# Kernel optimization log

Measured on AMD Instinct MI355X. Metric: run time of the kernel, lower is better.

Reference implementation:

```python
import jax, jax.numpy as jnp
import numpy as np

DIM = 1024
NUM_HEADS = 16
HEAD_DIM = DIM // NUM_HEADS


def setup_inputs() -> dict:
    key = jax.random.key(0)
    ks = jax.random.split(key, 8)
    B, N = 4, 1024
    x = jax.random.normal(ks[0], (B, N, DIM), dtype=jnp.float32)
    # RoPE tables per position, broadcast over batch/heads
    pos = jnp.arange(N, dtype=jnp.float32)[:, None]
    inv_freq = 1.0 / (10000.0 ** (jnp.arange(0, HEAD_DIM, 2, dtype=jnp.float32) / HEAD_DIM))
    ang = pos * inv_freq[None, :]                      # [N, D/2]
    ang = jnp.concatenate([ang, ang], axis=-1)          # [N, D]
    cos, sin = jnp.cos(ang), jnp.sin(ang)
    s_in = 1.0 / np.sqrt(DIM)
    qkv_w = jax.random.normal(ks[1], (3 * DIM, DIM), dtype=jnp.float32) * s_in
    qkv_b = jax.random.normal(ks[2], (3 * DIM,), dtype=jnp.float32) * 0.02
    proj_w = jax.random.normal(ks[3], (DIM, DIM), dtype=jnp.float32) * s_in
    proj_b = jax.random.normal(ks[4], (DIM,), dtype=jnp.float32) * 0.02
    return {"x": x, "cos": cos, "sin": sin, "qkv_w": qkv_w, "qkv_b": qkv_b,
            "proj_w": proj_w, "proj_b": proj_b}


def _rotate_half(t):
    t1, t2 = jnp.split(t, 2, axis=-1)
    return jnp.concatenate([-t2, t1], axis=-1)


def reference(x, cos, sin, qkv_w, qkv_b, proj_w, proj_b):
    B, N, C = x.shape
    H, D = NUM_HEADS, HEAD_DIM
    scale = D ** -0.5
    qkv = x @ qkv_w.T + qkv_b                           # [B, N, 3C]
    qkv = qkv.reshape(B, N, 3, H, D).transpose(2, 0, 3, 1, 4)  # [3, B, H, N, D]
    q, k, v = qkv[0], qkv[1], qkv[2]
    q = q * cos + _rotate_half(q) * sin                 # cos/sin [N, D] broadcast
    k = k * cos + _rotate_half(k) * sin
    attn = jnp.einsum('bhnd,bhmd->bhnm', q, k) * scale  # [B, H, N, N]
    attn = jax.nn.softmax(attn, axis=-1)
    out = jnp.einsum('bhnm,bhmd->bhnd', attn, v)        # [B, H, N, D]
    out = out.transpose(0, 2, 1, 3).reshape(B, N, C)
    return out @ proj_w.T + proj_b
```

## Files before the change

### kernel.cpp

```cpp
#include <hip/hip_runtime.h>

typedef __attribute__((ext_vector_type(8))) short bf16x8;
typedef __attribute__((ext_vector_type(4))) float f32x4;
typedef __attribute__((ext_vector_type(4))) unsigned short us4;

#define LOG2E 1.44269504088896f
#define GP(p) (const __attribute__((address_space(1))) void*)(p)
#define LP(p) (__attribute__((address_space(3))) void*)(p)

__device__ inline unsigned short f2bf(float f) {
    unsigned u = __float_as_uint(f);
    u += 0x7fffu + ((u >> 16) & 1u);
    return (unsigned short)(u >> 16);
}

__device__ inline unsigned cvt_pk_bf16(float lo, float hi) {
    unsigned r;
    asm("v_cvt_pk_bf16_f32 %0, %1, %2" : "=v"(r) : "v"(lo), "v"(hi));
    return r;
}

__global__ void cvt3_kernel(const float* __restrict__ x, const float* __restrict__ qw,
                            const float* __restrict__ pw,
                            unsigned short* __restrict__ xb, unsigned short* __restrict__ wqkv,
                            unsigned short* __restrict__ wproj) {
    const int nthreads = gridDim.x * blockDim.x;
    for (int i = blockIdx.x * blockDim.x + threadIdx.x; i < 2097152; i += nthreads) {
        const float* src; unsigned short* dst; int off;
        if (i < 1048576)      { src = x;  dst = xb;    off = i; }
        else if (i < 1835008) { src = qw; dst = wqkv;  off = i - 1048576; }
        else                  { src = pw; dst = wproj; off = i - 1835008; }
        const float4 v = *reinterpret_cast<const float4*>(src + off * 4);
        us4 o;
        o.x = f2bf(v.x); o.y = f2bf(v.y); o.z = f2bf(v.z); o.w = f2bf(v.w);
        *reinterpret_cast<us4*>(dst + off * 4) = o;
    }
}

__device__ inline void gemm_mainloop_db(const unsigned short* __restrict__ A,
                                        const unsigned short* __restrict__ Bw,
                                        unsigned short* As, unsigned short* Bs,
                                        int tm, int tn, f32x4 (&acc)[4][4]) {
    const int K = 1024;
    const int tid = threadIdx.x;
    const int lane = tid & 63;
    const int wv = tid >> 6;
    const int wr = wv >> 1, wc = wv & 1;
    const int lr = lane & 15, lg = lane >> 4;

    const int c1 = tid, c2 = tid + 256;
    const int r1 = c1 >> 2, r2 = c2 >> 2;
    const int g1 = ((c1 & 3) ^ ((r1 >> 1) & 3)) * 8;
    const int g2 = ((c2 & 3) ^ ((r2 >> 1) & 3)) * 8;
    const unsigned short* Ag1 = A + (size_t)(tm * 128 + r1) * K + g1;
    const unsigned short* Ag2 = A + (size_t)(tm * 128 + r2) * K + g2;
    const unsigned short* Bg1 = Bw + (size_t)(tn * 128 + r1) * K + g1;
    const unsigned short* Bg2 = Bw + (size_t)(tn * 128 + r2) * K + g2;

    const int rs = (lr >> 1) & 3;

    auto STAGE = [&](int buf, int k0) {
        __builtin_amdgcn_global_load_lds(GP(Ag1 + k0), LP(As + buf * 4096 + c1 * 8), 16, 0, 0);
        __builtin_amdgcn_global_load_lds(GP(Ag2 + k0), LP(As + buf * 4096 + c2 * 8), 16, 0, 0);
        __builtin_amdgcn_global_load_lds(GP(Bg1 + k0), LP(Bs + buf * 4096 + c1 * 8), 16, 0, 0);
        __builtin_amdgcn_global_load_lds(GP(Bg2 + k0), LP(Bs + buf * 4096 + c2 * 8), 16, 0, 0);
    };

    STAGE(0, 0);
    for (int t = 0; t < 32; t++) {
        const int buf = t & 1;
        if (t < 31) {
            STAGE(buf ^ 1, (t + 1) * 32);
            asm volatile("s_waitcnt vmcnt(4)" ::: "memory");
        } else {
            asm volatile("s_waitcnt vmcnt(0)" ::: "memory");
        }
        __builtin_amdgcn_s_barrier();
        __builtin_amdgcn_sched_barrier(0);

        bf16x8 af[4], bfv[4];
#pragma unroll
        for (int i = 0; i < 4; i++) {
            const int sl = (lg ^ rs) * 8;
            af[i]  = *reinterpret_cast<const bf16x8*>(As + buf * 4096 + (wr * 64 + i * 16 + lr) * 32 + sl);
            bfv[i] = *reinterpret_cast<const bf16x8*>(Bs + buf * 4096 + (wc * 64 + i * 16 + lr) * 32 + sl);
        }
        __builtin_amdgcn_s_setprio(1);
#pragma unroll
        for (int i = 0; i < 4; i++)
#pragma unroll
            for (int j = 0; j < 4; j++)
                acc[i][j] = __builtin_amdgcn_mfma_f32_16x16x32_bf16(af[i], bfv[j], acc[i][j], 0, 0, 0);
        __builtin_amdgcn_s_setprio(0);
        __builtin_amdgcn_s_barrier();
        __builtin_amdgcn_sched_barrier(0);
    }
}

__global__ __launch_bounds__(256, 4) void gemm_qkv_kernel(
        const unsigned short* __restrict__ A, const unsigned short* __restrict__ Bw,
        const float* __restrict__ bias, const float* __restrict__ cosT, const float* __restrict__ sinT,
        unsigned short* __restrict__ Qb, unsigned short* __restrict__ Kb, unsigned short* __restrict__ Vt) {
    __shared__ __align__(16) unsigned short As[2 * 4096];
    __shared__ __align__(16) unsigned short Bs[2 * 4096];
    const int tid = threadIdx.x;
    const int lane = tid & 63;
    const int wv = tid >> 6;
    const int wr = wv >> 1, wc = wv & 1;
    const int tm = blockIdx.y, tn = blockIdx.x;
    const int lr = lane & 15, lg = lane >> 4;

    f32x4 acc[4][4];
#pragma unroll
    for (int i = 0; i < 4; i++)
#pragma unroll
        for (int j = 0; j < 4; j++)
#pragma unroll
            for (int q = 0; q < 4; q++) acc[i][j][q] = 0.f;

    gemm_mainloop_db(A, Bw, As, Bs, tm, tn, acc);

    const int cbase = tn * 128 + wc * 64;
    const int sec = cbase >> 10;
    const int h = (cbase & 1023) >> 6;
    float bias_c[4];
#pragma unroll
    for (int j = 0; j < 4; j++) bias_c[j] = bias[cbase + j * 16 + lr];

    if (sec == 2) {
#pragma unroll
        for (int i = 0; i < 4; i++) {
            const int m0 = tm * 128 + wr * 64 + i * 16 + lg * 4;
            const int b = m0 >> 10, n0 = m0 & 1023;
#pragma unroll
            for (int j = 0; j < 4; j++) {
                const int d = j * 16 + lr;
                us4 pk;
                pk.x = f2bf(acc[i][j][0] + bias_c[j]); pk.y = f2bf(acc[i][j][1] + bias_c[j]);
                pk.z = f2bf(acc[i][j][2] + bias_c[j]); pk.w = f2bf(acc[i][j][3] + bias_c[j]);
                *reinterpret_cast<us4*>(Vt + ((size_t)((b * 16 + h) * 64 + d)) * 1024 + n0) = pk;
            }
        }
    } else {
#pragma unroll
        for (int i = 0; i < 4; i++) {
#pragma unroll
            for (int r = 0; r < 4; r++) {
                const int m = tm * 128 + wr * 64 + i * 16 + lg * 4 + r;
                const int b = m >> 10, n = m & 1023;
                float vals[4];
#pragma unroll
                for (int j = 0; j < 4; j++) vals[j] = acc[i][j][r] + bias_c[j];
#pragma unroll
                for (int j = 0; j < 4; j++) {
                    const int d = j * 16 + lr;
                    const float c = cosT[n * 64 + d];
                    const float s = sinT[n * 64 + d];
                    const float pr = vals[j ^ 2];
                    float outv = vals[j] * c + (d < 32 ? -pr : pr) * s;
                    if (sec == 0) outv *= 0.125f * LOG2E;
                    unsigned short* dst = (sec == 0) ? Qb : Kb;
                    dst[((size_t)((b * 16 + h) * 1024 + n)) * 64 + d] = f2bf(outv);
                }
            }
        }
    }
}

__global__ __launch_bounds__(256, 4) void attn_kernel(
        const unsigned short* __restrict__ Qb, const unsigned short* __restrict__ Kb,
        const unsigned short* __restrict__ Vt, unsigned short* __restrict__ AO) {
    __shared__ __align__(16) unsigned short Kbuf[2][4096];
    __shared__ __align__(16) unsigned short Vbuf[2][4096];
    const int tid = threadIdx.x, lane = tid & 63, wv = tid >> 6;
    const int bh = blockIdx.x, qt = blockIdx.y;
    const int qbase = qt * 64 + wv * 16;
    const unsigned short* Qp = Qb + (size_t)bh * 65536;
    const unsigned short* Kp = Kb + (size_t)bh * 65536;
    const unsigned short* Vp = Vt + (size_t)bh * 65536;
    const int lr = lane & 15, lg = lane >> 4;
    const int koff = (lr >> 2) * 8 + (lr & 3);

    const int s1 = tid, s2 = tid + 256;
    const int r1 = s1 >> 3, r2 = s2 >> 3;
    const int sc1 = (s1 & 7) ^ ((r1 & 3) | ((r1 >> 1) & 4));
    const int sc2 = (s2 & 7) ^ ((r2 & 3) | ((r2 >> 1) & 4));
    const unsigned short* Ks1 = Kp + r1 * 64 + sc1 * 8;
    const unsigned short* Ks2 = Kp + r2 * 64 + sc2 * 8;
    const unsigned short* Vs1 = Vp + r1 * 1024 + sc1 * 8;
    const unsigned short* Vs2 = Vp + r2 * 1024 + sc2 * 8;

    auto STAGE_K = [&](int buf, int kt) {
        __builtin_amdgcn_global_load_lds(GP(Ks1 + kt * 64), LP(&Kbuf[buf][0] + s1 * 8), 16, 0, 0);
        __builtin_amdgcn_global_load_lds(GP(Ks2 + kt * 64), LP(&Kbuf[buf][0] + s2 * 8), 16, 0, 0);
    };
    auto STAGE_V = [&](int buf, int kt) {
        __builtin_amdgcn_global_load_lds(GP(Vs1 + kt), LP(&Vbuf[buf][0] + s1 * 8), 16, 0, 0);
        __builtin_amdgcn_global_load_lds(GP(Vs2 + kt), LP(&Vbuf[buf][0] + s2 * 8), 16, 0, 0);
    };

    bf16x8 qfr[2];
#pragma unroll
    for (int kc = 0; kc < 2; kc++)
        qfr[kc] = *reinterpret_cast<const bf16x8*>(Qp + (qbase + lr) * 64 + kc * 32 + lg * 8);

    bf16x8 onesf;
#pragma unroll
    for (int j = 0; j < 8; j++) onesf[j] = (short)0x3F80;

    f32x4 o[4], l5;
#pragma unroll
    for (int df = 0; df < 4; df++)
#pragma unroll
        for (int r = 0; r < 4; r++) o[df][r] = 0.f;
#pragma unroll
    for (int r = 0; r < 4; r++) l5[r] = 0.f;

    auto QK = [&](f32x4 (&s)[4], const unsigned short* Kl) {
#pragma unroll
        for (int kf = 0; kf < 4; kf++)
#pragma unroll
            for (int r = 0; r < 4; r++) s[kf][r] = 0.f;
        __builtin_amdgcn_s_setprio(1);
#pragma unroll
        for (int kc = 0; kc < 2; kc++) {
#pragma unroll
            for (int kf = 0; kf < 4; kf++) {
                const int row = ((kf >> 1) << 5) + ((kf & 1) << 2) + koff;
                const int col = (kc * 4 + lg) ^ ((row & 3) | ((row >> 1) & 4));
                const bf16x8 kfr = *reinterpret_cast<const bf16x8*>(Kl + row * 64 + col * 8);
                s[kf] = __builtin_amdgcn_mfma_f32_16x16x32_bf16(kfr, qfr[kc], s[kf], 0, 0, 0);
            }
        }
        __builtin_amdgcn_s_setprio(0);
    };

    auto EXPpack = [&](f32x4 (&s)[4], bf16x8 (&pfr)[2]) {
#pragma unroll
        for (int kf = 0; kf < 4; kf++)
#pragma unroll
            for (int r = 0; r < 4; r++) s[kf][r] = exp2f(s[kf][r]);
#pragma unroll
        for (int kc = 0; kc < 2; kc++) {
            union { bf16x8 v; unsigned u[4]; } pk;
            pk.u[0] = cvt_pk_bf16(s[2 * kc][0], s[2 * kc][1]);
            pk.u[1] = cvt_pk_bf16(s[2 * kc][2], s[2 * kc][3]);
            pk.u[2] = cvt_pk_bf16(s[2 * kc + 1][0], s[2 * kc + 1][1]);
            pk.u[3] = cvt_pk_bf16(s[2 * kc + 1][2], s[2 * kc + 1][3]);
            pfr[kc] = pk.v;
        }
    };

    auto PV = [&](const unsigned short* Vl, bf16x8 (&pfr)[2]) {
        __builtin_amdgcn_s_setprio(1);
#pragma unroll
        for (int kc = 0; kc < 2; kc++) {
            l5 = __builtin_amdgcn_mfma_f32_16x16x32_bf16(onesf, pfr[kc], l5, 0, 0, 0);
#pragma unroll
            for (int df = 0; df < 4; df++) {
                const int vrow = df * 16 + lr;
                const int vcol = (kc * 4 + lg) ^ ((vrow & 3) | ((vrow >> 1) & 4));
                const bf16x8 vfr = *reinterpret_cast<const bf16x8*>(Vl + vrow * 64 + vcol * 8);
                o[df] = __builtin_amdgcn_mfma_f32_16x16x32_bf16(vfr, pfr[kc], o[df], 0, 0, 0);
            }
        }
        __builtin_amdgcn_s_setprio(0);
    };

    STAGE_K(0, 0);
    STAGE_K(1, 64);
    STAGE_V(0, 0);
    asm volatile("s_waitcnt vmcnt(0)" ::: "memory");
    __builtin_amdgcn_s_barrier();
    __builtin_amdgcn_sched_barrier(0);
    f32x4 sE[4], sO[4];
    QK(sE, &Kbuf[0][0]);

    bf16x8 pfr[2];
#pragma unroll 1
    for (int tt = 0; tt < 8; tt++) {
        const int t0 = 2 * tt, t1 = 2 * tt + 1;
        STAGE_K(0, (t0 + 2 < 16 ? t0 + 2 : 15) * 64);
        STAGE_V(1, t1 * 64);
        EXPpack(sE, pfr);
        asm volatile("s_waitcnt vmcnt(4)" ::: "memory");
        __builtin_amdgcn_s_barrier();
        __builtin_amdgcn_sched_barrier(0);
        QK(sO, &Kbuf[1][0]);
        PV(&Vbuf[0][0], pfr);
        __builtin_amdgcn_s_barrier();
        __builtin_amdgcn_sched_barrier(0);
        STAGE_K(1, (t1 + 2 < 16 ? t1 + 2 : 15) * 64);
        STAGE_V(0, (t1 + 1 < 16 ? t1 + 1 : 15) * 64);
        EXPpack(sO, pfr);
        asm volatile("s_waitcnt vmcnt(4)" ::: "memory");
        __builtin_amdgcn_s_barrier();
        __builtin_amdgcn_sched_barrier(0);
        if (tt < 7) QK(sE, &Kbuf[0][0]);
        PV(&Vbuf[1][0], pfr);
        __builtin_amdgcn_s_barrier();
        __builtin_amdgcn_sched_barrier(0);
    }

    const int b = bh >> 4, h = bh & 15;
    const float rinv = 1.f / l5[0];
    const int q = qbase + lr;
#pragma unroll
    for (int df = 0; df < 4; df++) {
        us4 pk;
        pk.x = f2bf(o[df][0] * rinv); pk.y = f2bf(o[df][1] * rinv);
        pk.z = f2bf(o[df][2] * rinv); pk.w = f2bf(o[df][3] * rinv);
        *reinterpret_cast<us4*>(AO + (size_t)(b * 1024 + q) * 1024 + h * 64 + df * 16 + lg * 4) = pk;
    }
}

__global__ __launch_bounds__(256, 3) void gemm_proj_kernel(
        const unsigned short* __restrict__ A, const unsigned short* __restrict__ Bw,
        const float* __restrict__ bias, float* __restrict__ out) {
    __shared__ __align__(16) unsigned short As[2 * 8192];
    __shared__ __align__(16) unsigned short Bs[2 * 4096];
    const int tid = threadIdx.x;
    const int lane = tid & 63;
    const int wv = tid >> 6;
    const int wr = wv >> 1, wc = wv & 1;
    const int tm = blockIdx.y, tn = blockIdx.x;
    const int lr = lane & 15, lg = lane >> 4;

    const unsigned short* Ag[4];
    const unsigned short* Bg[2];
    int doffA[4], doffB[2];
#pragma unroll
    for (int j = 0; j < 4; j++) {
        const int c = tid + j * 256;
        const int row = c >> 3, sl = c & 7;
        const int gs = (sl ^ ((row & 3) | ((row >> 1) & 4))) * 8;
        Ag[j] = A + (size_t)(tm * 128 + row) * 1024 + gs;
        doffA[j] = c * 8;
    }
#pragma unroll
    for (int j = 0; j < 2; j++) {
        const int c = tid + j * 256;
        const int row = c >> 3, sl = c & 7;
        const int gs = (sl ^ ((row & 3) | ((row >> 1) & 4))) * 8;
        Bg[j] = Bw + (size_t)(tn * 64 + row) * 1024 + gs;
        doffB[j] = c * 8;
    }

    f32x4 acc[4][2];
#pragma unroll
    for (int i = 0; i < 4; i++)
#pragma unroll
        for (int j = 0; j < 2; j++)
#pragma unroll
            for (int q = 0; q < 4; q++) acc[i][j][q] = 0.f;

    auto STAGE = [&](int buf, int k0) {
#pragma unroll
        for (int j = 0; j < 4; j++)
            __builtin_amdgcn_global_load_lds(GP(Ag[j] + k0), LP(As + buf * 8192 + doffA[j]), 16, 0, 0);
#pragma unroll
        for (int j = 0; j < 2; j++)
            __builtin_amdgcn_global_load_lds(GP(Bg[j] + k0), LP(Bs + buf * 4096 + doffB[j]), 16, 0, 0);
    };

    STAGE(0, 0);
    for (int t = 0; t < 16; t++) {
        const int buf = t & 1;
        if (t < 15) {
            STAGE(buf ^ 1, (t + 1) * 64);
            asm volatile("s_waitcnt vmcnt(6)" ::: "memory");
        } else {
            asm volatile("s_waitcnt vmcnt(0)" ::: "memory");
        }
        __builtin_amdgcn_s_barrier();
        __builtin_amdgcn_sched_barrier(0);

        bf16x8 af[4][2], bfv[2][2];
#pragma unroll
        for (int i = 0; i < 4; i++)
#pragma unroll
            for (int kk = 0; kk < 2; kk++) {
                const int ra = wr * 64 + i * 16 + lr;
                af[i][kk] = *reinterpret_cast<const bf16x8*>(
                    As + buf * 8192 + ra * 64 + ((kk * 4 + lg) ^ ((ra & 3) | ((ra >> 1) & 4))) * 8);
            }
#pragma unroll
        for (int j = 0; j < 2; j++)
#pragma unroll
            for (int kk = 0; kk < 2; kk++) {
                const int rb = wc * 32 + j * 16 + lr;
                bfv[j][kk] = *reinterpret_cast<const bf16x8*>(
                    Bs + buf * 4096 + rb * 64 + ((kk * 4 + lg) ^ ((rb & 3) | ((rb >> 1) & 4))) * 8);
            }
        __builtin_amdgcn_s_setprio(1);
#pragma unroll
        for (int i = 0; i < 4; i++)
#pragma unroll
            for (int j = 0; j < 2; j++)
#pragma unroll
                for (int kk = 0; kk < 2; kk++)
                    acc[i][j] = __builtin_amdgcn_mfma_f32_16x16x32_bf16(af[i][kk], bfv[j][kk], acc[i][j], 0, 0, 0);
        __builtin_amdgcn_s_setprio(0);
        __builtin_amdgcn_s_barrier();
        __builtin_amdgcn_sched_barrier(0);
    }

#pragma unroll
    for (int i = 0; i < 4; i++)
#pragma unroll
        for (int j = 0; j < 2; j++)
#pragma unroll
            for (int r = 0; r < 4; r++) {
                const int row = tm * 128 + wr * 64 + i * 16 + lg * 4 + r;
                const int col = tn * 64 + wc * 32 + j * 16 + lr;
                out[(size_t)row * 1024 + col] = acc[i][j][r] + bias[col];
            }
}

extern "C" void kernel_launch(void* const* d_in, const int* in_sizes, int n_in,
                              void* d_out, int out_size, void* d_ws, size_t ws_size,
                              hipStream_t stream) {
    const float* x      = (const float*)d_in[0];
    const float* cosT   = (const float*)d_in[1];
    const float* sinT   = (const float*)d_in[2];
    const float* qkv_w  = (const float*)d_in[3];
    const float* qkv_b  = (const float*)d_in[4];
    const float* proj_w = (const float*)d_in[5];
    const float* proj_b = (const float*)d_in[6];
    float* out = (float*)d_out;

    char* ws = (char*)d_ws;
    unsigned short* xb    = (unsigned short*)(ws);
    unsigned short* wqkv  = (unsigned short*)(ws + (8u << 20));
    unsigned short* wproj = (unsigned short*)(ws + (14u << 20));
    unsigned short* Qb    = (unsigned short*)(ws + (16u << 20));
    unsigned short* Kb    = (unsigned short*)(ws + (24u << 20));
    unsigned short* Vt    = (unsigned short*)(ws + (32u << 20));
    unsigned short* AO    = (unsigned short*)(ws + (40u << 20));

    cvt3_kernel<<<2048, 256, 0, stream>>>(x, qkv_w, proj_w, xb, wqkv, wproj);
    gemm_qkv_kernel<<<dim3(24, 32), 256, 0, stream>>>(xb, wqkv, qkv_b, cosT, sinT, Qb, Kb, Vt);
    attn_kernel<<<dim3(64, 16), 256, 0, stream>>>(Qb, Kb, Vt, AO);
    gemm_proj_kernel<<<dim3(16, 32), 256, 0, stream>>>(AO, wproj, proj_b, out);
}
```

Measured before the change: 94.04 us.

## Rewrite QKV GEMM as 256x256 tile with 8-wave phased K pipeline

Replaces the 128x128 double-buffered QKV GEMM mainloop with a 256x256 tile computed by 8 waves. K steps of 64 are split into half-tile phases, and each phase interleaves global-to-LDS staging of the next sub-tiles with MFMA work on the current ones. The aim is higher arithmetic intensity per LDS byte and better overlap of loads with compute. The grid shrinks to 192 blocks, fewer than the number of CUs, so some compute units sit idle. The new kernel also uses much more LDS and more registers.

```diff
diff --git a/kernel.cpp b/kernel.cpp
--- a/kernel.cpp
+++ b/kernel.cpp
@@ -37,127 +37,148 @@
     }
 }
 
-__device__ inline void gemm_mainloop_db(const unsigned short* __restrict__ A,
-                                        const unsigned short* __restrict__ Bw,
-                                        unsigned short* As, unsigned short* Bs,
-                                        int tm, int tn, f32x4 (&acc)[4][4]) {
-    const int K = 1024;
-    const int tid = threadIdx.x;
-    const int lane = tid & 63;
-    const int wv = tid >> 6;
-    const int wr = wv >> 1, wc = wv & 1;
-    const int lr = lane & 15, lg = lane >> 4;
-
-    const int c1 = tid, c2 = tid + 256;
-    const int r1 = c1 >> 2, r2 = c2 >> 2;
-    const int g1 = ((c1 & 3) ^ ((r1 >> 1) & 3)) * 8;
-    const int g2 = ((c2 & 3) ^ ((r2 >> 1) & 3)) * 8;
-    const unsigned short* Ag1 = A + (size_t)(tm * 128 + r1) * K + g1;
-    const unsigned short* Ag2 = A + (size_t)(tm * 128 + r2) * K + g2;
-    const unsigned short* Bg1 = Bw + (size_t)(tn * 128 + r1) * K + g1;
-    const unsigned short* Bg2 = Bw + (size_t)(tn * 128 + r2) * K + g2;
-
-    const int rs = (lr >> 1) & 3;
-
-    auto STAGE = [&](int buf, int k0) {
-        __builtin_amdgcn_global_load_lds(GP(Ag1 + k0), LP(As + buf * 4096 + c1 * 8), 16, 0, 0);
-        __builtin_amdgcn_global_load_lds(GP(Ag2 + k0), LP(As + buf * 4096 + c2 * 8), 16, 0, 0);
-        __builtin_amdgcn_global_load_lds(GP(Bg1 + k0), LP(Bs + buf * 4096 + c1 * 8), 16, 0, 0);
-        __builtin_amdgcn_global_load_lds(GP(Bg2 + k0), LP(Bs + buf * 4096 + c2 * 8), 16, 0, 0);
-    };
-
-    STAGE(0, 0);
-    for (int t = 0; t < 32; t++) {
-        const int buf = t & 1;
-        if (t < 31) {
-            STAGE(buf ^ 1, (t + 1) * 32);
-            asm volatile("s_waitcnt vmcnt(4)" ::: "memory");
-        } else {
-            asm volatile("s_waitcnt vmcnt(0)" ::: "memory");
-        }
-        __builtin_amdgcn_s_barrier();
-        __builtin_amdgcn_sched_barrier(0);
-
-        bf16x8 af[4], bfv[4];
-#pragma unroll
-        for (int i = 0; i < 4; i++) {
-            const int sl = (lg ^ rs) * 8;
-            af[i]  = *reinterpret_cast<const bf16x8*>(As + buf * 4096 + (wr * 64 + i * 16 + lr) * 32 + sl);
-            bfv[i] = *reinterpret_cast<const bf16x8*>(Bs + buf * 4096 + (wc * 64 + i * 16 + lr) * 32 + sl);
-        }
-        __builtin_amdgcn_s_setprio(1);
-#pragma unroll
-        for (int i = 0; i < 4; i++)
-#pragma unroll
-            for (int j = 0; j < 4; j++)
-                acc[i][j] = __builtin_amdgcn_mfma_f32_16x16x32_bf16(af[i], bfv[j], acc[i][j], 0, 0, 0);
-        __builtin_amdgcn_s_setprio(0);
-        __builtin_amdgcn_s_barrier();
-        __builtin_amdgcn_sched_barrier(0);
-    }
-}
-
-__global__ __launch_bounds__(256, 4) void gemm_qkv_kernel(
+__global__ __launch_bounds__(512, 2) void gemm_qkv_kernel(
         const unsigned short* __restrict__ A, const unsigned short* __restrict__ Bw,
         const float* __restrict__ bias, const float* __restrict__ cosT, const float* __restrict__ sinT,
         unsigned short* __restrict__ Qb, unsigned short* __restrict__ Kb, unsigned short* __restrict__ Vt) {
-    __shared__ __align__(16) unsigned short As[2 * 4096];
-    __shared__ __align__(16) unsigned short Bs[2 * 4096];
+    __shared__ __align__(16) unsigned short AL[2 * 16384];
+    __shared__ __align__(16) unsigned short BL[2 * 16384];
     const int tid = threadIdx.x;
-    const int lane = tid & 63;
-    const int wv = tid >> 6;
-    const int wr = wv >> 1, wc = wv & 1;
+    const int lane = tid & 63, wid = tid >> 6;
+    const int wm = wid >> 2, wn = wid & 3;
+    const int lr = lane & 15, lg = lane >> 4;
     const int tm = blockIdx.y, tn = blockIdx.x;
-    const int lr = lane & 15, lg = lane >> 4;
-
-    f32x4 acc[4][4];
-#pragma unroll
-    for (int i = 0; i < 4; i++)
+
+    const int srow = tid >> 3;
+    const int gslot = ((tid & 7) ^ (srow & 7)) * 8;
+    const int brow1 = (srow & 31) + ((srow >> 5) << 6);
+    const int brow2 = ((srow + 64) & 31) + (((srow + 64) >> 5) << 6);
+    const unsigned short* Agb = A + (size_t)tm * 256 * 1024;
+    const unsigned short* Bgb = Bw + (size_t)tn * 256 * 1024;
+
+    f32x4 acc[8][4];
+#pragma unroll
+    for (int i = 0; i < 8; i++)
 #pragma unroll
         for (int j = 0; j < 4; j++)
 #pragma unroll
             for (int q = 0; q < 4; q++) acc[i][j][q] = 0.f;
 
-    gemm_mainloop_db(A, Bw, As, Bs, tm, tn, acc);
-
-    const int cbase = tn * 128 + wc * 64;
+#define STGA(BUF, H, K0) do { \
+    const unsigned short* _s = Agb + (size_t)((H) * 64 + srow) * 1024 + (K0) + gslot; \
+    __builtin_amdgcn_global_load_lds(GP(_s), LP(AL + (BUF) * 16384 + (H) * 4096 + tid * 8), 16, 0, 0); \
+    __builtin_amdgcn_global_load_lds(GP(_s + 131072), LP(AL + (BUF) * 16384 + (H) * 4096 + 8192 + tid * 8), 16, 0, 0); \
+} while (0)
+#define STGB(BUF, H, K0) do { \
+    __builtin_amdgcn_global_load_lds(GP(Bgb + (size_t)(brow1 + (H) * 32) * 1024 + (K0) + gslot), \
+        LP(BL + (BUF) * 16384 + (brow1 + (H) * 32) * 64 + (tid & 7) * 8), 16, 0, 0); \
+    __builtin_amdgcn_global_load_lds(GP(Bgb + (size_t)(brow2 + (H) * 32) * 1024 + (K0) + gslot), \
+        LP(BL + (BUF) * 16384 + (brow2 + (H) * 32) * 64 + (tid & 7) * 8), 16, 0, 0); \
+} while (0)
+
+#define PH(BUF, MH, NH, STG_STMT, VM) do { \
+    bf16x8 paf[4][2], pbf[2][2]; \
+    const unsigned short* _Ab = AL + (BUF) * 16384; \
+    const unsigned short* _Bb = BL + (BUF) * 16384; \
+    _Pragma("unroll") \
+    for (int mr = 0; mr < 4; mr++) \
+        _Pragma("unroll") \
+        for (int kk = 0; kk < 2; kk++) { \
+            const int rw = wm * 128 + (MH) * 64 + mr * 16 + lr; \
+            paf[mr][kk] = *reinterpret_cast<const bf16x8*>(_Ab + rw * 64 + ((kk * 4 + lg) ^ (rw & 7)) * 8); \
+        } \
+    _Pragma("unroll") \
+    for (int nf = 0; nf < 2; nf++) \
+        _Pragma("unroll") \
+        for (int kk = 0; kk < 2; kk++) { \
+            const int rw = wn * 64 + (NH) * 32 + nf * 16 + lr; \
+            pbf[nf][kk] = *reinterpret_cast<const bf16x8*>(_Bb + rw * 64 + ((kk * 4 + lg) ^ (rw & 7)) * 8); \
+        } \
+    STG_STMT; \
+    __builtin_amdgcn_s_barrier(); \
+    asm volatile("s_waitcnt lgkmcnt(0)" ::: "memory"); \
+    __builtin_amdgcn_sched_barrier(0); \
+    __builtin_amdgcn_s_setprio(1); \
+    _Pragma("unroll") \
+    for (int mr = 0; mr < 4; mr++) \
+        _Pragma("unroll") \
+        for (int nf = 0; nf < 2; nf++) \
+            _Pragma("unroll") \
+            for (int kk = 0; kk < 2; kk++) \
+                acc[(MH) * 4 + mr][(NH) * 2 + nf] = __builtin_amdgcn_mfma_f32_16x16x32_bf16( \
+                    paf[mr][kk], pbf[nf][kk], acc[(MH) * 4 + mr][(NH) * 2 + nf], 0, 0, 0); \
+    __builtin_amdgcn_s_setprio(0); \
+    if (VM) asm volatile("s_waitcnt vmcnt(4)" ::: "memory"); \
+    __builtin_amdgcn_s_barrier(); \
+    __builtin_amdgcn_sched_barrier(0); \
+} while (0)
+
+    STGA(0, 0, 0);
+    STGB(0, 1, 0);
+    STGA(0, 1, 0);
+    STGB(0, 0, 0);
+    STGA(1, 0, 64);
+    STGB(1, 1, 64);
+    asm volatile("s_waitcnt vmcnt(4)" ::: "memory");
+    __builtin_amdgcn_s_barrier();
+    __builtin_amdgcn_sched_barrier(0);
+
+#pragma unroll 1
+    for (int i = 0; i < 8; i++) {
+        const int t1k = (2 * i + 1) * 64;
+        const int t2k = (2 * i + 2 < 16 ? 2 * i + 2 : 15) * 64;
+        const int t3k = (2 * i + 3 < 16 ? 2 * i + 3 : 15) * 64;
+        PH(0, 0, 0, STGA(1, 1, t1k), 0);
+        PH(0, 0, 1, STGB(1, 0, t1k), 0);
+        PH(0, 1, 1, STGA(0, 0, t2k), 0);
+        PH(0, 1, 0, STGB(0, 1, t2k), 1);
+        PH(1, 0, 0, STGA(0, 1, t2k), 0);
+        PH(1, 0, 1, STGB(0, 0, t2k), 0);
+        PH(1, 1, 1, STGA(1, 0, t3k), 0);
+        PH(1, 1, 0, STGB(1, 1, t3k), 1);
+    }
+#undef PH
+#undef STGA
+#undef STGB
+
+    const int cbase = tn * 256 + wn * 64;
     const int sec = cbase >> 10;
     const int h = (cbase & 1023) >> 6;
     float bias_c[4];
 #pragma unroll
-    for (int j = 0; j < 4; j++) bias_c[j] = bias[cbase + j * 16 + lr];
+    for (int nf = 0; nf < 4; nf++) bias_c[nf] = bias[cbase + nf * 16 + lr];
 
     if (sec == 2) {
 #pragma unroll
-        for (int i = 0; i < 4; i++) {
-            const int m0 = tm * 128 + wr * 64 + i * 16 + lg * 4;
+        for (int mr8 = 0; mr8 < 8; mr8++) {
+            const int m0 = tm * 256 + wm * 128 + mr8 * 16 + lg * 4;
             const int b = m0 >> 10, n0 = m0 & 1023;
 #pragma unroll
-            for (int j = 0; j < 4; j++) {
-                const int d = j * 16 + lr;
+            for (int nf = 0; nf < 4; nf++) {
+                const int d = nf * 16 + lr;
                 us4 pk;
-                pk.x = f2bf(acc[i][j][0] + bias_c[j]); pk.y = f2bf(acc[i][j][1] + bias_c[j]);
-                pk.z = f2bf(acc[i][j][2] + bias_c[j]); pk.w = f2bf(acc[i][j][3] + bias_c[j]);
+                pk.x = f2bf(acc[mr8][nf][0] + bias_c[nf]); pk.y = f2bf(acc[mr8][nf][1] + bias_c[nf]);
+                pk.z = f2bf(acc[mr8][nf][2] + bias_c[nf]); pk.w = f2bf(acc[mr8][nf][3] + bias_c[nf]);
                 *reinterpret_cast<us4*>(Vt + ((size_t)((b * 16 + h) * 64 + d)) * 1024 + n0) = pk;
             }
         }
     } else {
 #pragma unroll
-        for (int i = 0; i < 4; i++) {
+        for (int mr8 = 0; mr8 < 8; mr8++) {
 #pragma unroll
             for (int r = 0; r < 4; r++) {
-                const int m = tm * 128 + wr * 64 + i * 16 + lg * 4 + r;
+                const int m = tm * 256 + wm * 128 + mr8 * 16 + lg * 4 + r;
                 const int b = m >> 10, n = m & 1023;
                 float vals[4];
 #pragma unroll
-                for (int j = 0; j < 4; j++) vals[j] = acc[i][j][r] + bias_c[j];
-#pragma unroll
-                for (int j = 0; j < 4; j++) {
-                    const int d = j * 16 + lr;
+                for (int nf = 0; nf < 4; nf++) vals[nf] = acc[mr8][nf][r] + bias_c[nf];
+#pragma unroll
+                for (int nf = 0; nf < 4; nf++) {
+                    const int d = nf * 16 + lr;
                     const float c = cosT[n * 64 + d];
                     const float s = sinT[n * 64 + d];
-                    const float pr = vals[j ^ 2];
-                    float outv = vals[j] * c + (d < 32 ? -pr : pr) * s;
+                    const float pr = vals[nf ^ 2];
+                    float outv = vals[nf] * c + (d < 32 ? -pr : pr) * s;
                     if (sec == 0) outv *= 0.125f * LOG2E;
                     unsigned short* dst = (sec == 0) ? Qb : Kb;
                     dst[((size_t)((b * 16 + h) * 1024 + n)) * 64 + d] = f2bf(outv);
@@ -439,7 +460,7 @@
     unsigned short* AO    = (unsigned short*)(ws + (40u << 20));
 
     cvt3_kernel<<<2048, 256, 0, stream>>>(x, qkv_w, proj_w, xb, wqkv, wproj);
-    gemm_qkv_kernel<<<dim3(24, 32), 256, 0, stream>>>(xb, wqkv, qkv_b, cosT, sinT, Qb, Kb, Vt);
+    gemm_qkv_kernel<<<dim3(12, 16), 512, 0, stream>>>(xb, wqkv, qkv_b, cosT, sinT, Qb, Kb, Vt);
     attn_kernel<<<dim3(64, 16), 256, 0, stream>>>(Qb, Kb, Vt, AO);
     gemm_proj_kernel<<<dim3(16, 32), 256, 0, stream>>>(AO, wproj, proj_b, out);
 }
```

Result: slower. 102.8 us (+9.3%).
